# Kernel tuning notes

Hardware: AMD Instinct MI355X
Metric: run time of the kernel (lower is better)

## Reference

```python
import jax, jax.numpy as jnp
import numpy as np

N, D = 16384, 256


def setup_inputs() -> dict:
    key = jax.random.key(0)
    k1, k2 = jax.random.split(key)
    # L2-normalized features as produced by CLIP/SigLIP towers
    img = jax.random.normal(k1, (N, D), dtype=jnp.float32)
    txt = jax.random.normal(k2, (N, D), dtype=jnp.float32)
    img = img / jnp.linalg.norm(img, axis=-1, keepdims=True)
    txt = txt / jnp.linalg.norm(txt, axis=-1, keepdims=True)
    return {
        "image_features": img,
        "text_features": txt,
        "logit_scale": jnp.float32(10.0),   # exp(log(10)) per SigLIP init
        "logit_bias": jnp.float32(-10.0),   # SigLIP init
    }


def reference(image_features, text_features, logit_scale, logit_bias):
    n = image_features.shape[0]
    # [N, N] logits = scale * img @ txt.T + bias
    logits = logit_scale * jnp.matmul(image_features, text_features.T) + logit_bias
    # labels: +1 on diagonal, -1 off-diagonal
    labels = 2.0 * jnp.eye(n, dtype=logits.dtype) - 1.0
    loss = -jnp.sum(jax.nn.log_sigmoid(labels * logits)) / n
    return loss
```

## Files before the change

### kernel.cpp

```cpp
#include <hip/hip_runtime.h>
#include <stdint.h>

constexpr int kN = 16384;
constexpr int kD = 256;
constexpr int TM = 256, TN = 256;
constexpr int KB = kD / 2;

using floatx16 = __attribute__((ext_vector_type(16))) float;
using floatx2  = __attribute__((ext_vector_type(2))) float;
using intx2v   = __attribute__((ext_vector_type(2))) int;
using intx4    = __attribute__((ext_vector_type(4))) int;
using intx8    = __attribute__((ext_vector_type(8))) int;

__device__ __forceinline__ uint32_t q4(float x) {
    float y = fabsf(x * 16.f);
    uint32_t c = (y >= 0.25f) + (y >= 0.75f) + (y >= 1.25f) + (y >= 1.75f)
               + (y >= 2.5f)  + (y >= 3.5f)  + (y >= 5.0f);
    return c | (x < 0.f ? 8u : 0u);
}

__global__ __launch_bounds__(256)
void cvt_fp4_kernel(const float* __restrict__ a, const float* __restrict__ b,
                    unsigned int* __restrict__ oa, unsigned int* __restrict__ ob,
                    float* __restrict__ out) {
    int idx = blockIdx.x * 256 + threadIdx.x;
    if (idx == 0) *out = 0.f;
    float4 a0 = *(const float4*)(a + (size_t)idx * 8);
    float4 a1 = *(const float4*)(a + (size_t)idx * 8 + 4);
    float4 b0 = *(const float4*)(b + (size_t)idx * 8);
    float4 b1 = *(const float4*)(b + (size_t)idx * 8 + 4);
    uint32_t pa = q4(a0.x) | (q4(a0.y) << 4) | (q4(a0.z) << 8)  | (q4(a0.w) << 12)
                | (q4(a1.x) << 16) | (q4(a1.y) << 20) | (q4(a1.z) << 24) | (q4(a1.w) << 28);
    uint32_t pb = q4(b0.x) | (q4(b0.y) << 4) | (q4(b0.z) << 8)  | (q4(b0.w) << 12)
                | (q4(b1.x) << 16) | (q4(b1.y) << 20) | (q4(b1.z) << 24) | (q4(b1.w) << 28);
    oa[idx] = pa;
    ob[idx] = pb;
}

#define CAT8(lo, hi) __builtin_shufflevector((lo), (hi), 0, 1, 2, 3, 4, 5, 6, 7)
#define ROT8(v)      __builtin_shufflevector((v), (v), 4, 5, 6, 7, -1, -1, -1, -1)

__global__ __launch_bounds__(512, 2)
void siglip_gemm_loss_kernel(const unsigned char* __restrict__ A,
                             const unsigned char* __restrict__ B,
                             const float* __restrict__ scale_p,
                             const float* __restrict__ bias_p,
                             float* __restrict__ out) {
    __shared__ float red[8];

    const int tid  = threadIdx.x;
    const int wave = tid >> 6;
    const int lane = tid & 63;

    const int g    = blockIdx.x;
    const int tRow = ((g & 7) << 3) + (g >> 5);
    const int sCol = (g >> 3) & 3;

    const int wr = wave >> 2, wc = wave & 3;
    const int m0 = wr * 128, n0 = wc * 64;
    const int l31 = lane & 31;
    const int h   = lane >> 5;

    const float sc  = *scale_p * (1.0f / 256.0f);
    const float bs  = *bias_p;
    const float sc3 = sc * (1.44269504f * 8388608.0f);
    const float bs3 = fmaf(bs, 1.44269504f * 8388608.0f, 1064986823.0f);
    const floatx2 sc3v = (floatx2)(sc3);
    const floatx2 bs3v = (floatx2)(bs3);

    intx8 af8[4][2];
    #pragma unroll
    for (int i = 0; i < 4; ++i) {
        const unsigned char* pa = A + ((size_t)tRow * TM + m0 + i * 32 + l31) * KB + 16 * h;
        #pragma unroll
        for (int p = 0; p < 2; ++p) {
            const intx4 lo = *(const intx4*)(pa + (2 * p) * 32);
            const intx4 hi = *(const intx4*)(pa + (2 * p + 1) * 32);
            af8[i][p] = CAT8(lo, hi);
        }
    }

    const floatx16 z16 = (floatx16)(0.f);

    floatx16 acc[2][2];
    floatx2 sm0 = (floatx2)(0.f), sm1 = (floatx2)(0.f);
    float smd = 0.f;

    const unsigned char* pb = B + (size_t)sCol * TN * KB;
    const int voff0 = (n0 + l31) * KB + 16 * h;
    const int voff1 = voff0 + 32 * KB;
    const size_t tStride = (size_t)4 * TN * KB;

    intx8 bl[2][2];

    auto loadTile = [&]() {
        #pragma unroll
        for (int j = 0; j < 2; ++j) {
            const int vo = j ? voff1 : voff0;
            #pragma unroll
            for (int p = 0; p < 2; ++p) {
                const intx4 lo = *(const intx4*)(pb + vo + (2 * p) * 32);
                const intx4 hi = *(const intx4*)(pb + vo + (2 * p + 1) * 32);
                bl[j][p] = CAT8(lo, hi);
            }
        }
        pb += tStride;
    };

    auto mfmaHalf = [&](const int ibase) {
        __builtin_amdgcn_s_setprio(1);
        #pragma unroll
        for (int p = 0; p < 2; ++p) {
            #pragma unroll
            for (int ii = 0; ii < 2; ++ii) {
                const intx8 a = af8[ibase + ii][p];
                #pragma unroll
                for (int j = 0; j < 2; ++j)
                    acc[ii][j] = __builtin_amdgcn_mfma_scale_f32_32x32x64_f8f6f4(
                        a, bl[j][p], p == 0 ? z16 : acc[ii][j],
                        4 , 4 ,
                        0, 127, 0, 127 );
            }
            const intx8 br0 = ROT8(bl[0][p]);
            const intx8 br1 = ROT8(bl[1][p]);
            #pragma unroll
            for (int ii = 0; ii < 2; ++ii) {
                const intx8 a = ROT8(af8[ibase + ii][p]);
                acc[ii][0] = __builtin_amdgcn_mfma_scale_f32_32x32x64_f8f6f4(
                    a, br0, acc[ii][0], 4, 4, 0, 127, 0, 127);
                acc[ii][1] = __builtin_amdgcn_mfma_scale_f32_32x32x64_f8f6f4(
                    a, br1, acc[ii][1], 4, 4, 0, 127, 0, 127);
            }
        }
        __builtin_amdgcn_s_setprio(0);
    };

    auto epiHalf = [&](const int ibase, const int tCol) {
        #pragma unroll
        for (int ii = 0; ii < 2; ++ii)
            #pragma unroll
            for (int j = 0; j < 2; ++j) {
                const floatx16 a = acc[ii][j];
                #pragma unroll
                for (int v = 0; v < 16; v += 4) {
                    floatx2 t0 = {a[v + 0], a[v + 1]};
                    floatx2 t1 = {a[v + 2], a[v + 3]};
                    t0 = __builtin_elementwise_fma(t0, sc3v, bs3v);
                    t1 = __builtin_elementwise_fma(t1, sc3v, bs3v);
                    const intx2v e0 = {(int)t0.x, (int)t0.y};
                    const intx2v e1 = {(int)t1.x, (int)t1.y};
                    sm0 += __builtin_bit_cast(floatx2, e0);
                    sm1 += __builtin_bit_cast(floatx2, e1);
                }
                const int gRow0 = tRow * TM + m0 + (ibase + ii) * 32;
                const int gCol0 = tCol * TN + n0 + j * 32;
                if (gRow0 == gCol0) {
                    #pragma unroll
                    for (int v = 0; v < 16; ++v) {
                        const int rrow = (v & 3) + 8 * (v >> 2) + 4 * h;
                        if (rrow == l31)
                            smd += fmaf(a[v], sc, bs);
                    }
                }
            }
    };

    loadTile();
    mfmaHalf(0);
    epiHalf(0, sCol);
    mfmaHalf(2);
    for (int s = 1; s < 16; ++s) {
        loadTile();
        epiHalf(2, sCol + 4 * (s - 1));
        mfmaHalf(0);
        epiHalf(0, sCol + 4 * s);
        mfmaHalf(2);
    }
    epiHalf(2, sCol + 60);

    float sum = (sm0.x + sm1.x) + (sm0.y + sm1.y) - smd;

    #pragma unroll
    for (int off = 32; off > 0; off >>= 1)
        sum += __shfl_down(sum, off);
    if (lane == 0) red[wave] = sum;
    __syncthreads();
    if (tid == 0) {
        float s2 = 0.f;
        #pragma unroll
        for (int w = 0; w < 8; ++w) s2 += red[w];
        atomicAdd(out, s2 * (1.0f / (float)kN));
    }
}

extern "C" void kernel_launch(void* const* d_in, const int* in_sizes, int n_in,
                              void* d_out, int out_size, void* d_ws, size_t ws_size,
                              hipStream_t stream) {
    const float* img     = (const float*)d_in[0];
    const float* txt     = (const float*)d_in[1];
    const float* scale_p = (const float*)d_in[2];
    const float* bias_p  = (const float*)d_in[3];
    float* out = (float*)d_out;

    unsigned char* Af4 = (unsigned char*)d_ws;
    unsigned char* Bf4 = Af4 + (size_t)kN * KB;

    cvt_fp4_kernel<<<dim3(kN * kD / 8 / 256), dim3(256), 0, stream>>>(
        img, txt, (unsigned int*)Af4, (unsigned int*)Bf4, out);
    siglip_gemm_loss_kernel<<<dim3(256), dim3(512), 0, stream>>>(
        Af4, Bf4, scale_p, bias_p, out);
}
```

Measured before the change: 121.2 us.

## Double-buffer B tile loads and split fp4 operand registers into 16-byte pieces

```diff
diff --git a/kernel.cpp b/kernel.cpp
--- a/kernel.cpp
+++ b/kernel.cpp
@@ -37,8 +37,9 @@
     ob[idx] = pb;
 }
 
-#define CAT8(lo, hi) __builtin_shufflevector((lo), (hi), 0, 1, 2, 3, 4, 5, 6, 7)
-#define ROT8(v)      __builtin_shufflevector((v), (v), 4, 5, 6, 7, -1, -1, -1, -1)
+#define U8(v)  __builtin_shufflevector((v), (v), 0, 1, 2, 3, -1, -1, -1, -1)
+#define MFMA4(a, b, c) __builtin_amdgcn_mfma_scale_f32_32x32x64_f8f6f4( \
+        (a), (b), (c), 4 , 4 , 0, 127, 0, 127)
 
 __global__ __launch_bounds__(512, 2)
 void siglip_gemm_loss_kernel(const unsigned char* __restrict__ A,
@@ -61,6 +62,8 @@
     const int l31 = lane & 31;
     const int h   = lane >> 5;
 
+    if (wr) __builtin_amdgcn_s_sleep(10);
+
     const float sc  = *scale_p * (1.0f / 256.0f);
     const float bs  = *bias_p;
     const float sc3 = sc * (1.44269504f * 8388608.0f);
@@ -68,16 +71,13 @@
     const floatx2 sc3v = (floatx2)(sc3);
     const floatx2 bs3v = (floatx2)(bs3);
 
-    intx8 af8[4][2];
+    intx4 af[4][4];
     #pragma unroll
     for (int i = 0; i < 4; ++i) {
         const unsigned char* pa = A + ((size_t)tRow * TM + m0 + i * 32 + l31) * KB + 16 * h;
         #pragma unroll
-        for (int p = 0; p < 2; ++p) {
-            const intx4 lo = *(const intx4*)(pa + (2 * p) * 32);
-            const intx4 hi = *(const intx4*)(pa + (2 * p + 1) * 32);
-            af8[i][p] = CAT8(lo, hi);
-        }
+        for (int q = 0; q < 4; ++q)
+            af[i][q] = *(const intx4*)(pa + q * 32);
     }
 
     const floatx16 z16 = (floatx16)(0.f);
@@ -91,51 +91,34 @@
     const int voff1 = voff0 + 32 * KB;
     const size_t tStride = (size_t)4 * TN * KB;
 
-    intx8 bl[2][2];
+    intx4 blA[2][4], blB[2][4];
 
-    auto loadTile = [&]() {
+    auto loadT = [&](intx4 (&bl)[2][4]) {
         #pragma unroll
         for (int j = 0; j < 2; ++j) {
             const int vo = j ? voff1 : voff0;
             #pragma unroll
-            for (int p = 0; p < 2; ++p) {
-                const intx4 lo = *(const intx4*)(pb + vo + (2 * p) * 32);
-                const intx4 hi = *(const intx4*)(pb + vo + (2 * p + 1) * 32);
-                bl[j][p] = CAT8(lo, hi);
-            }
+            for (int q = 0; q < 4; ++q)
+                bl[j][q] = *(const intx4*)(pb + vo + q * 32);
         }
         pb += tStride;
     };
 
-    auto mfmaHalf = [&](const int ibase) {
-        __builtin_amdgcn_s_setprio(1);
+    auto mfmaH = [&](const intx4 (&bq)[2][4], const int ibase) {
         #pragma unroll
-        for (int p = 0; p < 2; ++p) {
+        for (int q = 0; q < 4; ++q) {
             #pragma unroll
             for (int ii = 0; ii < 2; ++ii) {
-                const intx8 a = af8[ibase + ii][p];
+                const intx8 a = U8(af[ibase + ii][q]);
                 #pragma unroll
                 for (int j = 0; j < 2; ++j)
-                    acc[ii][j] = __builtin_amdgcn_mfma_scale_f32_32x32x64_f8f6f4(
-                        a, bl[j][p], p == 0 ? z16 : acc[ii][j],
-                        4 , 4 ,
-                        0, 127, 0, 127 );
-            }
-            const intx8 br0 = ROT8(bl[0][p]);
-            const intx8 br1 = ROT8(bl[1][p]);
-            #pragma unroll
-            for (int ii = 0; ii < 2; ++ii) {
-                const intx8 a = ROT8(af8[ibase + ii][p]);
-                acc[ii][0] = __builtin_amdgcn_mfma_scale_f32_32x32x64_f8f6f4(
-                    a, br0, acc[ii][0], 4, 4, 0, 127, 0, 127);
-                acc[ii][1] = __builtin_amdgcn_mfma_scale_f32_32x32x64_f8f6f4(
-                    a, br1, acc[ii][1], 4, 4, 0, 127, 0, 127);
+                    acc[ii][j] = MFMA4(a, U8(bq[j][q]),
+                                       q == 0 ? z16 : acc[ii][j]);
             }
         }
-        __builtin_amdgcn_s_setprio(0);
     };
 
-    auto epiHalf = [&](const int ibase, const int tCol) {
+    auto epiH = [&](const int ibase, const int tCol) {
         #pragma unroll
         for (int ii = 0; ii < 2; ++ii)
             #pragma unroll
@@ -158,25 +141,28 @@
                     #pragma unroll
                     for (int v = 0; v < 16; ++v) {
                         const int rrow = (v & 3) + 8 * (v >> 2) + 4 * h;
-                        if (rrow == l31)
-                            smd += fmaf(a[v], sc, bs);
+                        if (rrow == l31) smd += fmaf(a[v], sc, bs);
                     }
                 }
             }
     };
 
-    loadTile();
-    mfmaHalf(0);
-    epiHalf(0, sCol);
-    mfmaHalf(2);
+    loadT(blA);
+    loadT(blB);
+    mfmaH(blA, 0);
+    epiH(0, sCol);
+    mfmaH(blA, 2);
+    loadT(blA);
     for (int s = 1; s < 16; ++s) {
-        loadTile();
-        epiHalf(2, sCol + 4 * (s - 1));
-        mfmaHalf(0);
-        epiHalf(0, sCol + 4 * s);
-        mfmaHalf(2);
+        const intx4 (&cur)[2][4] = (s & 1) ? blB : blA;
+        const int cPrev = sCol + 4 * (s - 1);
+        epiH(2, cPrev);
+        mfmaH(cur, 0);
+        epiH(0, cPrev + 4);
+        mfmaH(cur, 2);
+        if (s < 14) loadT((s & 1) ? blB : blA);
     }
-    epiHalf(2, sCol + 60);
+    epiH(2, sCol + 60);
 
     float sum = (sm0.x + sm1.x) + (sm0.y + sm1.y) - smd;
 
```

Measured after the change: 221.8 us. 1.83x slower.
